# Performance work log

Measured on AMD Instinct MI355X. Metric: run time of the kernel, lower is better.

Reference implementation:

```python
import jax, jax.numpy as jnp
import numpy as np

H = 8  # num_heads (hidden_size=512 -> head dim 64)

def setup_inputs() -> dict:
    key = jax.random.key(0)
    ks = jax.random.split(key, 14)
    B, D, N, S, L = 16, 512, 128, 14, 12
    f = lambda k, shp: jax.random.normal(k, shp, dtype=jnp.float32)
    return {
        "q": f(ks[0], (B, D, N, S)),
        "k": f(ks[1], (B, D, N, S)),
        "v": f(ks[2], (B, D, N, S)),
        "attn_bias": f(ks[3], (B, L, N, N, H)),
        "Wq": f(ks[4], (D, D)) * 0.02, "bq": f(ks[5], (D,)) * 0.02,
        "Wk": f(ks[6], (D, D)) * 0.02, "bk": f(ks[7], (D,)) * 0.02,
        "Wv": f(ks[8], (D, D)) * 0.02, "bv": f(ks[9], (D,)) * 0.02,
        "Wd": f(ks[10], (S, L)) * 0.02, "bd": f(ks[11], (S,)) * 0.02,  # Dimension1: in_len->14
        "Wo": f(ks[12], (D, D)) * 0.02, "bo": f(ks[13], (D,)) * 0.02,
    }


def reference(q, k, v, attn_bias, Wq, bq, Wk, bk, Wv, bv, Wd, bd, Wo, bo):
    B, D, N, S = q.shape
    d = D // H
    scale = d ** -0.5
    # transpose(1,3): [B,D,N,S] -> [B,S,N,D]
    qt = jnp.transpose(q, (0, 3, 2, 1))
    kt = jnp.transpose(k, (0, 3, 2, 1))
    vt = jnp.transpose(v, (0, 3, 2, 1))
    # linear projections + split heads: [B,S,N,H,d] -> [B,S,H,N,d]
    qh = (qt @ Wq.T + bq).reshape(B, S, N, H, d).transpose(0, 1, 3, 2, 4) * scale
    kh = (kt @ Wk.T + bk).reshape(B, S, N, H, d).transpose(0, 1, 3, 2, 4)
    vh = (vt @ Wv.T + bv).reshape(B, S, N, H, d).transpose(0, 1, 3, 2, 4)
    # scores over node axis: [B,S,H,N,N]
    scores = jnp.einsum('bshnd,bshmd->bshnm', qh, kh)
    # bias: [B,L,N,N,H] -(Linear over L)-> [B,S,N,N,H] -> [B,S,H,N,N]
    bias = jnp.einsum('blnmh,sl->bsnmh', attn_bias, Wd) + bd[None, :, None, None, None]
    scores = scores + jnp.transpose(bias, (0, 1, 4, 2, 3))
    # NOTE: original uses softmax over dim=3 (the query/node-row axis) - kept faithful
    attn = jax.nn.softmax(scores, axis=3)
    out = jnp.einsum('bshnm,bshmd->bshnd', attn, vh)
    out = jnp.transpose(out, (0, 1, 3, 2, 4)).reshape(B, S, N, D)
    # output projection (dropout is identity at inference)
    return out @ Wo.T + bo
```

## Files before the change

kernel.cpp:

```cpp
#include <hip/hip_runtime.h>


typedef unsigned short u16;
typedef __bf16 bf16x8 __attribute__((ext_vector_type(8)));
typedef float f32x4 __attribute__((ext_vector_type(4)));

__device__ __forceinline__ u16 f2bf(float f) {
  unsigned u = __float_as_uint(f);
  u += 0x7fffu + ((u >> 16) & 1u);
  return (u16)(u >> 16);
}
__device__ __forceinline__ float bf2f(u16 b) {
  return __uint_as_float(((unsigned)b) << 16);
}

__global__ __launch_bounds__(256) void wconv_kernel(const float* __restrict__ Wq, const float* __restrict__ Wk,
                                                    const float* __restrict__ Wv, const float* __restrict__ Wo,
                                                    u16* __restrict__ wbf) {
  int idx = (blockIdx.x * 256 + threadIdx.x) * 4;
  int m = idx >> 18;
  int r = idx & 262143;
  const float* src = (m == 0) ? Wq : (m == 1) ? Wk : (m == 2) ? Wv : Wo;
  float sc = (m == 0) ? 0.125f : 1.0f;
  float4 v = *(const float4*)&src[r];
  ushort4 o;
  o.x = f2bf(v.x * sc); o.y = f2bf(v.y * sc); o.z = f2bf(v.z * sc); o.w = f2bf(v.w * sc);
  *(ushort4*)&wbf[idx] = o;
}

__global__ __launch_bounds__(256) void transpose_kernel(const float* __restrict__ q, const float* __restrict__ k,
                                                        const float* __restrict__ v, u16* __restrict__ xT) {
  __shared__ u16 tile[64 * 76];
  const int nst = blockIdx.x;
  const int dt  = blockIdx.y;
  const int z   = blockIdx.z;
  const int which = z >> 4, b = z & 15;
  const float* src = (which == 0) ? q : (which == 1) ? k : v;
  u16* dst = xT + which * 14680064;
  const int t = threadIdx.x;
  const int c4 = t & 15, r0 = t >> 4;
#pragma unroll
  for (int it = 0; it < 4; ++it) {
    int r = r0 + it * 16;
    float4 f = *(const float4*)&src[(b * 512 + dt * 64 + r) * 1792 + nst * 64 + c4 * 4];
    ushort4 o; o.x = f2bf(f.x); o.y = f2bf(f.y); o.z = f2bf(f.z); o.w = f2bf(f.w);
    *(ushort4*)&tile[r * 76 + c4 * 4] = o;
  }
  __syncthreads();
  const int dq = t & 15, nr0 = t >> 4;
#pragma unroll
  for (int it = 0; it < 4; ++it) {
    int nr = nr0 + it * 16;
    ushort4 o;
    o.x = tile[(dq * 4 + 0) * 76 + nr];
    o.y = tile[(dq * 4 + 1) * 76 + nr];
    o.z = tile[(dq * 4 + 2) * 76 + nr];
    o.w = tile[(dq * 4 + 3) * 76 + nr];
    *(ushort4*)&dst[(b * 1792 + nst * 64 + nr) * 512 + dt * 64 + dq * 4] = o;
  }
}

__device__ __forceinline__ void gemm128(const u16* __restrict__ Ag, const u16* __restrict__ Bg,
                                        u16* sA, u16* sB, f32x4 acc[2][8]) {
  const int t = threadIdx.x;
  const int w = t >> 6, l = t & 63;
  const int lw = l >> 4, ll16 = l & 15;
  for (int kb = 0; kb < 8; ++kb) {
#pragma unroll
    for (int it = 0; it < 4; ++it) {
      int i = t + 256 * it;
      int row = i >> 3, g = i & 7;
      int so = ((g >> 2) << 12) + row * 32 + (g & 3) * 8;
      int go = row * 512 + kb * 64 + g * 8;
      *(uint4*)&sA[so] = *(const uint4*)&Ag[go];
      *(uint4*)&sB[so] = *(const uint4*)&Bg[go];
    }
    __syncthreads();
#pragma unroll
    for (int kk = 0; kk < 2; ++kk) {
      const int ko = (kk << 12) + lw * 8;
      bf16x8 a0 = *(const bf16x8*)&sA[ko + (w * 32 + ll16) * 32];
      bf16x8 a1 = *(const bf16x8*)&sA[ko + (w * 32 + 16 + ll16) * 32];
#pragma unroll
      for (int mt = 0; mt < 8; ++mt) {
        bf16x8 bb = *(const bf16x8*)&sB[ko + (mt * 16 + ll16) * 32];
        acc[0][mt] = __builtin_amdgcn_mfma_f32_16x16x32_bf16(a0, bb, acc[0][mt], 0, 0, 0);
        acc[1][mt] = __builtin_amdgcn_mfma_f32_16x16x32_bf16(a1, bb, acc[1][mt], 0, 0, 0);
      }
    }
    __syncthreads();
  }
}

__global__ __launch_bounds__(256) void proj_kernel(const u16* __restrict__ xT, const u16* __restrict__ wbf,
                                                   const float* __restrict__ bq, const float* __restrict__ bk,
                                                   const float* __restrict__ bv, u16* __restrict__ qh) {
  __shared__ u16 sA[8192], sB[8192];
  const int bx = blockIdx.x;
  const int by = blockIdx.y;
  const int z  = blockIdx.z;
  const int p = z >> 4, b = z & 15;
  const u16* Ag = xT + p * 14680064 + b * 917504 + by * 65536;
  const u16* Bg = wbf + p * 262144 + bx * 65536;
  const float* bvec = (p == 0) ? bq : (p == 1) ? bk : bv;
  const float bscale = (p == 0) ? 0.125f : 1.0f;
  u16* outp = qh + p * 14680064;

  f32x4 acc[2][8];
#pragma unroll
  for (int i = 0; i < 2; ++i)
#pragma unroll
    for (int j = 0; j < 8; ++j)
#pragma unroll
      for (int e = 0; e < 4; ++e) acc[i][j][e] = 0.f;

  gemm128(Ag, Bg, sA, sB, acc);

  const int t = threadIdx.x, w = t >> 6, l = t & 63;
  const int lw = l >> 4, ll16 = l & 15;
#pragma unroll
  for (int mt = 0; mt < 8; ++mt) {
    int e = bx * 128 + mt * 16 + ll16;
    float bias = bvec[e] * bscale;
    int hh = e >> 6, dd = e & 63;
#pragma unroll
    for (int nt = 0; nt < 2; ++nt) {
#pragma unroll
      for (int j = 0; j < 4; ++j) {
        unsigned row = by * 128 + w * 32 + nt * 16 + lw * 4 + j;
        unsigned n = row / 14u;
        unsigned sI = row - n * 14u;
        outp[(((b * 14 + sI) * 8 + hh) << 13) + n * 64 + dd] = f2bf(acc[nt][mt][j] + bias);
      }
    }
  }
}

__global__ __launch_bounds__(256) void bias_kernel(const float* __restrict__ ab, const float* __restrict__ Wd,
                                                   const float* __restrict__ bd, u16* __restrict__ biasws) {
  __shared__ float abt[12 * 520];
  __shared__ float sWd[168];
  __shared__ float sbd[14];
  const int m0 = blockIdx.x * 64;
  const int n  = blockIdx.y;
  const int b  = blockIdx.z;
  const int t = threadIdx.x;
  if (t < 168) sWd[t] = Wd[t];
  if (t < 14)  sbd[t] = bd[t];
#pragma unroll
  for (int it = 0; it < 24; ++it) {
    int i = t + 256 * it;
    int lI = i >> 9, rem = i & 511;
    int m = rem >> 3, hI = rem & 7;
    float v = ab[((b * 12 + lI) * 16384 + n * 128 + m0 + m) * 8 + hI];
    abt[lI * 520 + hI * 65 + m] = v;
  }
  __syncthreads();
  const int m = t & 63, qq = t >> 6;
#pragma unroll
  for (int hh = 0; hh < 2; ++hh) {
    int h = qq * 2 + hh;
    float v[12];
#pragma unroll
    for (int lI = 0; lI < 12; ++lI) v[lI] = abt[lI * 520 + h * 65 + m];
#pragma unroll
    for (int sI = 0; sI < 14; ++sI) {
      float r = sbd[sI];
#pragma unroll
      for (int lI = 0; lI < 12; ++lI) r += v[lI] * sWd[sI * 12 + lI];
      biasws[((b * 14 + sI) * 8 + h) * 16384 + n * 128 + m0 + m] = f2bf(r);
    }
  }
}

__global__ __launch_bounds__(256) void attn_kernel(const u16* __restrict__ qh, const u16* __restrict__ kh,
                                                   const u16* __restrict__ vh, const u16* __restrict__ biasws,
                                                   u16* __restrict__ attn_out) {
  __shared__ u16 smem[24576];
  u16* sQ = smem;
  u16* sK = smem + 8192;
  u16* sV = smem + 16384;
  u16* sP = smem;

  const int sI = blockIdx.x, h = blockIdx.y, b = blockIdx.z;
  const int t = threadIdx.x, w = t >> 6, l = t & 63;
  const int lw = l >> 4, ll16 = l & 15;
  const int bsh = ((b * 14 + sI) * 8 + h) << 13;

#pragma unroll
  for (int it = 0; it < 4; ++it) {
    int i = t + 256 * it;
    int row = i >> 3, g = i & 7;
    int so = ((g >> 2) << 12) + row * 32 + (g & 3) * 8;
    *(uint4*)&sQ[so] = *(const uint4*)&qh[bsh + row * 64 + g * 8];
    *(uint4*)&sK[so] = *(const uint4*)&kh[bsh + row * 64 + g * 8];
  }
#pragma unroll
  for (int it = 0; it < 4; ++it) {
    int m = (t >> 3) + 32 * it;
    int dd0 = (t & 7) * 8;
    uint4 u = *(const uint4*)&vh[bsh + m * 64 + dd0];
    const u16* pu = (const u16*)&u;
    int mo = (m >> 3) * 512 + (m & 7);
#pragma unroll
    for (int j = 0; j < 8; ++j) {
      int d = dd0 + j;
      sV[mo + (d >> 4) * 128 + (d & 15) * 8] = pu[j];
    }
  }
  __syncthreads();

  f32x4 acc[8][2];
  const int mb = w * 32;
#pragma unroll
  for (int nt = 0; nt < 8; ++nt)
#pragma unroll
    for (int mtl = 0; mtl < 2; ++mtl)
#pragma unroll
      for (int j = 0; j < 4; ++j)
        acc[nt][mtl][j] = bf2f(biasws[(bsh << 1) + (nt * 16 + lw * 4 + j) * 128 + mb + mtl * 16 + ll16]);

#pragma unroll
  for (int ks = 0; ks < 2; ++ks) {
    const int ko = (ks << 12) + lw * 8;
    bf16x8 b0 = *(const bf16x8*)&sK[ko + (mb + ll16) * 32];
    bf16x8 b1 = *(const bf16x8*)&sK[ko + (mb + 16 + ll16) * 32];
#pragma unroll
    for (int nt = 0; nt < 8; ++nt) {
      bf16x8 a = *(const bf16x8*)&sQ[ko + (nt * 16 + ll16) * 32];
      acc[nt][0] = __builtin_amdgcn_mfma_f32_16x16x32_bf16(a, b0, acc[nt][0], 0, 0, 0);
      acc[nt][1] = __builtin_amdgcn_mfma_f32_16x16x32_bf16(a, b1, acc[nt][1], 0, 0, 0);
    }
  }

  float inv[2];
#pragma unroll
  for (int mtl = 0; mtl < 2; ++mtl) {
    float mx = -3.0e38f;
#pragma unroll
    for (int nt = 0; nt < 8; ++nt)
#pragma unroll
      for (int j = 0; j < 4; ++j) mx = fmaxf(mx, acc[nt][mtl][j]);
    mx = fmaxf(mx, __shfl_xor(mx, 16));
    mx = fmaxf(mx, __shfl_xor(mx, 32));
    float sum = 0.f;
#pragma unroll
    for (int nt = 0; nt < 8; ++nt)
#pragma unroll
      for (int j = 0; j < 4; ++j) {
        float e = __expf(acc[nt][mtl][j] - mx);
        acc[nt][mtl][j] = e;
        sum += e;
      }
    sum += __shfl_xor(sum, 16);
    sum += __shfl_xor(sum, 32);
    inv[mtl] = 1.0f / sum;
  }

  __syncthreads();

#pragma unroll
  for (int nt = 0; nt < 8; ++nt)
#pragma unroll
    for (int mtl = 0; mtl < 2; ++mtl)
#pragma unroll
      for (int j = 0; j < 4; ++j)
        sP[(w << 12) + (nt * 16 + lw * 4 + j) * 32 + mtl * 16 + ll16] = f2bf(acc[nt][mtl][j] * inv[mtl]);

  __syncthreads();

  f32x4 o[2][4];
#pragma unroll
  for (int i = 0; i < 2; ++i)
#pragma unroll
    for (int dt2 = 0; dt2 < 4; ++dt2)
#pragma unroll
      for (int e = 0; e < 4; ++e) o[i][dt2][e] = 0.f;
#pragma unroll
  for (int ks = 0; ks < 4; ++ks) {
    const int ko = (ks << 12) + lw * 8;
    bf16x8 a0 = *(const bf16x8*)&sP[ko + ((w * 2 + 0) * 16 + ll16) * 32];
    bf16x8 a1 = *(const bf16x8*)&sP[ko + ((w * 2 + 1) * 16 + ll16) * 32];
#pragma unroll
    for (int dt2 = 0; dt2 < 4; ++dt2) {
      bf16x8 bv2 = *(const bf16x8*)&sV[(ks * 4 + lw) * 512 + dt2 * 128 + ll16 * 8];
      o[0][dt2] = __builtin_amdgcn_mfma_f32_16x16x32_bf16(a0, bv2, o[0][dt2], 0, 0, 0);
      o[1][dt2] = __builtin_amdgcn_mfma_f32_16x16x32_bf16(a1, bv2, o[1][dt2], 0, 0, 0);
    }
  }

  const int ob = ((b * 14 + sI) * 128) * 512 + h * 64;
#pragma unroll
  for (int t2 = 0; t2 < 2; ++t2)
#pragma unroll
    for (int dt2 = 0; dt2 < 4; ++dt2)
#pragma unroll
      for (int j = 0; j < 4; ++j) {
        int rn = w * 32 + t2 * 16 + lw * 4 + j;
        attn_out[ob + rn * 512 + dt2 * 16 + ll16] = f2bf(o[t2][dt2][j]);
      }
}

__global__ __launch_bounds__(256) void out_kernel(const u16* __restrict__ attn_out, const u16* __restrict__ wobf,
                                                  const float* __restrict__ bo, float* __restrict__ out) {
  __shared__ u16 sA[8192], sB[8192];
  const int bx = blockIdx.x;
  const int by = blockIdx.y;
  f32x4 acc[2][8];
#pragma unroll
  for (int i = 0; i < 2; ++i)
#pragma unroll
    for (int j = 0; j < 8; ++j)
#pragma unroll
      for (int e = 0; e < 4; ++e) acc[i][j][e] = 0.f;

  gemm128(attn_out + by * 65536, wobf + bx * 65536, sA, sB, acc);

  const int t = threadIdx.x, w = t >> 6, l = t & 63;
  const int lw = l >> 4, ll16 = l & 15;
#pragma unroll
  for (int mt = 0; mt < 8; ++mt) {
    int e = bx * 128 + mt * 16 + ll16;
    float bias = bo[e];
#pragma unroll
    for (int nt = 0; nt < 2; ++nt) {
#pragma unroll
      for (int j = 0; j < 4; ++j) {
        int row = by * 128 + w * 32 + nt * 16 + lw * 4 + j;
        out[row * 512 + e] = acc[nt][mt][j] + bias;
      }
    }
  }
}

extern "C" void kernel_launch(void* const* d_in, const int* in_sizes, int n_in,
                              void* d_out, int out_size, void* d_ws, size_t ws_size,
                              hipStream_t stream) {
  (void)in_sizes; (void)n_in; (void)out_size; (void)ws_size;
  const float* q  = (const float*)d_in[0];
  const float* k  = (const float*)d_in[1];
  const float* v  = (const float*)d_in[2];
  const float* ab = (const float*)d_in[3];
  const float* Wq = (const float*)d_in[4];
  const float* bq = (const float*)d_in[5];
  const float* Wk = (const float*)d_in[6];
  const float* bk = (const float*)d_in[7];
  const float* Wv = (const float*)d_in[8];
  const float* bv = (const float*)d_in[9];
  const float* Wd = (const float*)d_in[10];
  const float* bd = (const float*)d_in[11];
  const float* Wo = (const float*)d_in[12];
  const float* bo = (const float*)d_in[13];
  float* out = (float*)d_out;

  u16* ws = (u16*)d_ws;
  u16* xT      = ws;
  u16* qh      = ws + 44040192;
  u16* wbf     = ws + 88080384;
  u16* biasws  = ws;
  u16* attnout = ws + 29360128;

  wconv_kernel<<<dim3(1024), dim3(256), 0, stream>>>(Wq, Wk, Wv, Wo, wbf);
  transpose_kernel<<<dim3(28, 8, 48), dim3(256), 0, stream>>>(q, k, v, xT);
  proj_kernel<<<dim3(4, 14, 48), dim3(256), 0, stream>>>(xT, wbf, bq, bk, bv, qh);
  bias_kernel<<<dim3(2, 128, 16), dim3(256), 0, stream>>>(ab, Wd, bd, biasws);
  attn_kernel<<<dim3(14, 8, 16), dim3(256), 0, stream>>>(qh, qh + 14680064, qh + 29360128, biasws, attnout);
  out_kernel<<<dim3(4, 224), dim3(256), 0, stream>>>(attnout, wbf + 786432, bo, out);
}
```

Baseline: 477.6 us.

## Use direct global-to-LDS loads, XCD-aware block mapping, and coalesced bias/output layouts

GEMM tile loads in the projection and output GEMMs, and the Q/K loads in attention, now use global_load_lds, which writes global memory straight into LDS instead of going through registers. Grid indices for the projection and output kernels are remapped so neighbouring tiles land on the same XCD for better L2 reuse. The transpose now writes rows in s-major order, which makes the projection epilogue write contiguously. The bias kernel writes a [b,n,s,h,m] layout with vectorised loads and stores, and attention stages both the bias and its output tile through LDS so global accesses are coalesced. In exchange, attention uses more LDS and adds extra barriers.

```diff
diff --git a/kernel.cpp b/kernel.cpp
--- a/kernel.cpp
+++ b/kernel.cpp
@@ -4,6 +4,10 @@
 typedef unsigned short u16;
 typedef __bf16 bf16x8 __attribute__((ext_vector_type(8)));
 typedef float f32x4 __attribute__((ext_vector_type(4)));
+
+#define GLDS16(g, l) __builtin_amdgcn_global_load_lds( \
+    (const __attribute__((address_space(1))) void*)(g), \
+    (__attribute__((address_space(3))) void*)(l), 16, 0, 0)
 
 __device__ __forceinline__ u16 f2bf(float f) {
   unsigned u = __float_as_uint(f);
@@ -51,12 +55,14 @@
 #pragma unroll
   for (int it = 0; it < 4; ++it) {
     int nr = nr0 + it * 16;
+    unsigned c = nst * 64 + nr;
+    unsigned n = c / 14u, sI = c - n * 14u;
     ushort4 o;
     o.x = tile[(dq * 4 + 0) * 76 + nr];
     o.y = tile[(dq * 4 + 1) * 76 + nr];
     o.z = tile[(dq * 4 + 2) * 76 + nr];
     o.w = tile[(dq * 4 + 3) * 76 + nr];
-    *(ushort4*)&dst[(b * 1792 + nst * 64 + nr) * 512 + dt * 64 + dq * 4] = o;
+    *(ushort4*)&dst[(b * 1792 + sI * 128 + n) * 512 + dt * 64 + dq * 4] = o;
   }
 }
 
@@ -68,12 +74,12 @@
   for (int kb = 0; kb < 8; ++kb) {
 #pragma unroll
     for (int it = 0; it < 4; ++it) {
-      int i = t + 256 * it;
-      int row = i >> 3, g = i & 7;
-      int so = ((g >> 2) << 12) + row * 32 + (g & 3) * 8;
+      int c = w * 64 + it * 256 + l;
+      int row = (c >> 2) & 127;
+      int g = ((c >> 9) << 2) | (c & 3);
       int go = row * 512 + kb * 64 + g * 8;
-      *(uint4*)&sA[so] = *(const uint4*)&Ag[go];
-      *(uint4*)&sB[so] = *(const uint4*)&Bg[go];
+      GLDS16(Ag + go, sA + (w * 64 + it * 256) * 8);
+      GLDS16(Bg + go, sB + (w * 64 + it * 256) * 8);
     }
     __syncthreads();
 #pragma unroll
@@ -96,9 +102,12 @@
                                                    const float* __restrict__ bq, const float* __restrict__ bk,
                                                    const float* __restrict__ bv, u16* __restrict__ qh) {
   __shared__ u16 sA[8192], sB[8192];
-  const int bx = blockIdx.x;
-  const int by = blockIdx.y;
-  const int z  = blockIdx.z;
+  const unsigned u = blockIdx.x;
+  const int xcd = u & 7, slot = u >> 3;
+  const int bx = slot & 3;
+  const int gidx = xcd * 84 + (slot >> 2);
+  const int by = gidx % 14;
+  const int z  = gidx / 14;
   const int p = z >> 4, b = z & 15;
   const u16* Ag = xT + p * 14680064 + b * 917504 + by * 65536;
   const u16* Bg = wbf + p * 262144 + bx * 65536;
@@ -127,60 +136,57 @@
     for (int nt = 0; nt < 2; ++nt) {
 #pragma unroll
       for (int j = 0; j < 4; ++j) {
-        unsigned row = by * 128 + w * 32 + nt * 16 + lw * 4 + j;
-        unsigned n = row / 14u;
-        unsigned sI = row - n * 14u;
-        outp[(((b * 14 + sI) * 8 + hh) << 13) + n * 64 + dd] = f2bf(acc[nt][mt][j] + bias);
+        int n = w * 32 + nt * 16 + lw * 4 + j;
+        outp[(((b * 14 + by) * 8 + hh) << 13) + n * 64 + dd] = f2bf(acc[nt][mt][j] + bias);
       }
     }
   }
 }
 
 __global__ __launch_bounds__(256) void bias_kernel(const float* __restrict__ ab, const float* __restrict__ Wd,
-                                                   const float* __restrict__ bd, u16* __restrict__ biasws) {
-  __shared__ float abt[12 * 520];
-  __shared__ float sWd[168];
-  __shared__ float sbd[14];
-  const int m0 = blockIdx.x * 64;
-  const int n  = blockIdx.y;
-  const int b  = blockIdx.z;
+                                                   const float* __restrict__ bd, u16* __restrict__ bias2) {
+  __shared__ float abt[12 * 1056];
+  const int n = blockIdx.x;
+  const int b = blockIdx.y;
   const int t = threadIdx.x;
-  if (t < 168) sWd[t] = Wd[t];
-  if (t < 14)  sbd[t] = bd[t];
-#pragma unroll
-  for (int it = 0; it < 24; ++it) {
+#pragma unroll
+  for (int it = 0; it < 12; ++it) {
     int i = t + 256 * it;
-    int lI = i >> 9, rem = i & 511;
-    int m = rem >> 3, hI = rem & 7;
-    float v = ab[((b * 12 + lI) * 16384 + n * 128 + m0 + m) * 8 + hI];
-    abt[lI * 520 + hI * 65 + m] = v;
-  }
-  __syncthreads();
-  const int m = t & 63, qq = t >> 6;
-#pragma unroll
-  for (int hh = 0; hh < 2; ++hh) {
-    int h = qq * 2 + hh;
-    float v[12];
-#pragma unroll
-    for (int lI = 0; lI < 12; ++lI) v[lI] = abt[lI * 520 + h * 65 + m];
-#pragma unroll
-    for (int sI = 0; sI < 14; ++sI) {
-      float r = sbd[sI];
-#pragma unroll
-      for (int lI = 0; lI < 12; ++lI) r += v[lI] * sWd[sI * 12 + lI];
-      biasws[((b * 14 + sI) * 8 + h) * 16384 + n * 128 + m0 + m] = f2bf(r);
-    }
+    int lI = i >> 8, rem = i & 255;
+    int m = rem >> 1, hq = rem & 1;
+    float4 f = *(const float4*)&ab[(((b * 12 + lI) * 128 + n) * 128 + m) * 8 + hq * 4];
+    float* dstp = &abt[lI * 1056 + (hq * 4) * 132 + m];
+    dstp[0] = f.x; dstp[132] = f.y; dstp[264] = f.z; dstp[396] = f.w;
+  }
+  __syncthreads();
+  const int h = t >> 5, m0 = (t & 31) * 4;
+  float4 f4[12];
+#pragma unroll
+  for (int lI = 0; lI < 12; ++lI) f4[lI] = *(const float4*)&abt[lI * 1056 + h * 132 + m0];
+  u16* outb = bias2 + (b * 128 + n) * 14336 + h * 128 + m0;
+#pragma unroll
+  for (int sI = 0; sI < 14; ++sI) {
+    float r0 = bd[sI], r1 = bd[sI], r2 = bd[sI], r3 = bd[sI];
+#pragma unroll
+    for (int lI = 0; lI < 12; ++lI) {
+      float wv = Wd[sI * 12 + lI];
+      r0 += wv * f4[lI].x; r1 += wv * f4[lI].y; r2 += wv * f4[lI].z; r3 += wv * f4[lI].w;
+    }
+    ushort4 o; o.x = f2bf(r0); o.y = f2bf(r1); o.z = f2bf(r2); o.w = f2bf(r3);
+    *(ushort4*)&outb[sI * 1024] = o;
   }
 }
 
 __global__ __launch_bounds__(256) void attn_kernel(const u16* __restrict__ qh, const u16* __restrict__ kh,
-                                                   const u16* __restrict__ vh, const u16* __restrict__ biasws,
+                                                   const u16* __restrict__ vh, const u16* __restrict__ bias2,
                                                    u16* __restrict__ attn_out) {
-  __shared__ u16 smem[24576];
+  __shared__ u16 smem[25600];
+  u16* sBias = smem;
   u16* sQ = smem;
   u16* sK = smem + 8192;
-  u16* sV = smem + 16384;
   u16* sP = smem;
+  u16* sOut = smem;
+  u16* sV = smem + 17408;
 
   const int sI = blockIdx.x, h = blockIdx.y, b = blockIdx.z;
   const int t = threadIdx.x, w = t >> 6, l = t & 63;
@@ -189,18 +195,10 @@
 
 #pragma unroll
   for (int it = 0; it < 4; ++it) {
-    int i = t + 256 * it;
-    int row = i >> 3, g = i & 7;
-    int so = ((g >> 2) << 12) + row * 32 + (g & 3) * 8;
-    *(uint4*)&sQ[so] = *(const uint4*)&qh[bsh + row * 64 + g * 8];
-    *(uint4*)&sK[so] = *(const uint4*)&kh[bsh + row * 64 + g * 8];
-  }
-#pragma unroll
-  for (int it = 0; it < 4; ++it) {
     int m = (t >> 3) + 32 * it;
     int dd0 = (t & 7) * 8;
-    uint4 u = *(const uint4*)&vh[bsh + m * 64 + dd0];
-    const u16* pu = (const u16*)&u;
+    uint4 uu = *(const uint4*)&vh[bsh + m * 64 + dd0];
+    const u16* pu = (const u16*)&uu;
     int mo = (m >> 3) * 512 + (m & 7);
 #pragma unroll
     for (int j = 0; j < 8; ++j) {
@@ -208,6 +206,16 @@
       sV[mo + (d >> 4) * 128 + (d & 15) * 8] = pu[j];
     }
   }
+  {
+    const u16* bb = bias2 + (b * 128) * 14336 + sI * 1024 + h * 128;
+#pragma unroll
+    for (int it = 0; it < 8; ++it) {
+      int c = t + 256 * it;
+      int n = c >> 4, mc = c & 15;
+      uint4 uu = *(const uint4*)&bb[n * 14336 + mc * 8];
+      *(uint4*)&sBias[n * 136 + mc * 8] = uu;
+    }
+  }
   __syncthreads();
 
   f32x4 acc[8][2];
@@ -218,7 +226,19 @@
     for (int mtl = 0; mtl < 2; ++mtl)
 #pragma unroll
       for (int j = 0; j < 4; ++j)
-        acc[nt][mtl][j] = bf2f(biasws[(bsh << 1) + (nt * 16 + lw * 4 + j) * 128 + mb + mtl * 16 + ll16]);
+        acc[nt][mtl][j] = bf2f(sBias[(nt * 16 + lw * 4 + j) * 136 + mb + mtl * 16 + ll16]);
+  __syncthreads();
+
+#pragma unroll
+  for (int it = 0; it < 4; ++it) {
+    int c = w * 64 + it * 256 + l;
+    int row = (c >> 2) & 127;
+    int g = ((c >> 9) << 2) | (c & 3);
+    int go = row * 64 + g * 8;
+    GLDS16(qh + bsh + go, sQ + (w * 64 + it * 256) * 8);
+    GLDS16(kh + bsh + go, sK + (w * 64 + it * 256) * 8);
+  }
+  __syncthreads();
 
 #pragma unroll
   for (int ks = 0; ks < 2; ++ks) {
@@ -256,7 +276,6 @@
     sum += __shfl_xor(sum, 32);
     inv[mtl] = 1.0f / sum;
   }
-
   __syncthreads();
 
 #pragma unroll
@@ -266,7 +285,6 @@
 #pragma unroll
       for (int j = 0; j < 4; ++j)
         sP[(w << 12) + (nt * 16 + lw * 4 + j) * 32 + mtl * 16 + ll16] = f2bf(acc[nt][mtl][j] * inv[mtl]);
-
   __syncthreads();
 
   f32x4 o[2][4];
@@ -288,8 +306,8 @@
       o[1][dt2] = __builtin_amdgcn_mfma_f32_16x16x32_bf16(a1, bv2, o[1][dt2], 0, 0, 0);
     }
   }
-
-  const int ob = ((b * 14 + sI) * 128) * 512 + h * 64;
+  __syncthreads();
+
 #pragma unroll
   for (int t2 = 0; t2 < 2; ++t2)
 #pragma unroll
@@ -297,15 +315,26 @@
 #pragma unroll
       for (int j = 0; j < 4; ++j) {
         int rn = w * 32 + t2 * 16 + lw * 4 + j;
-        attn_out[ob + rn * 512 + dt2 * 16 + ll16] = f2bf(o[t2][dt2][j]);
-      }
+        sOut[rn * 72 + dt2 * 16 + ll16] = f2bf(o[t2][dt2][j]);
+      }
+  __syncthreads();
+  const int ob = ((b * 14 + sI) * 128) * 512 + h * 64;
+#pragma unroll
+  for (int i = 0; i < 4; ++i) {
+    int c = t + 256 * i;
+    int row = c >> 3, ch = c & 7;
+    uint4 uu = *(const uint4*)&sOut[row * 72 + ch * 8];
+    *(uint4*)&attn_out[ob + row * 512 + ch * 8] = uu;
+  }
 }
 
 __global__ __launch_bounds__(256) void out_kernel(const u16* __restrict__ attn_out, const u16* __restrict__ wobf,
                                                   const float* __restrict__ bo, float* __restrict__ out) {
   __shared__ u16 sA[8192], sB[8192];
-  const int bx = blockIdx.x;
-  const int by = blockIdx.y;
+  const unsigned u = blockIdx.x;
+  const int xcd = u & 7, slot = u >> 3;
+  const int bx = slot & 3;
+  const int by = xcd * 28 + (slot >> 2);
   f32x4 acc[2][8];
 #pragma unroll
   for (int i = 0; i < 2; ++i)
@@ -357,13 +386,13 @@
   u16* xT      = ws;
   u16* qh      = ws + 44040192;
   u16* wbf     = ws + 88080384;
-  u16* biasws  = ws;
+  u16* bias2   = ws;
   u16* attnout = ws + 29360128;
 
   wconv_kernel<<<dim3(1024), dim3(256), 0, stream>>>(Wq, Wk, Wv, Wo, wbf);
   transpose_kernel<<<dim3(28, 8, 48), dim3(256), 0, stream>>>(q, k, v, xT);
-  proj_kernel<<<dim3(4, 14, 48), dim3(256), 0, stream>>>(xT, wbf, bq, bk, bv, qh);
-  bias_kernel<<<dim3(2, 128, 16), dim3(256), 0, stream>>>(ab, Wd, bd, biasws);
-  attn_kernel<<<dim3(14, 8, 16), dim3(256), 0, stream>>>(qh, qh + 14680064, qh + 29360128, biasws, attnout);
-  out_kernel<<<dim3(4, 224), dim3(256), 0, stream>>>(attnout, wbf + 786432, bo, out);
-}
+  proj_kernel<<<dim3(2688), dim3(256), 0, stream>>>(xT, wbf, bq, bk, bv, qh);
+  bias_kernel<<<dim3(128, 16), dim3(256), 0, stream>>>(ab, Wd, bd, bias2);
+  attn_kernel<<<dim3(14, 8, 16), dim3(256), 0, stream>>>(qh, qh + 14680064, qh + 29360128, bias2, attnout);
+  out_kernel<<<dim3(896), dim3(256), 0, stream>>>(attnout, wbf + 786432, bo, out);
+}
```

After: 464.5 us. 1.03x faster.
